# Kernel optimization log

Measured on AMD Instinct MI355X. Metric: run time of the kernel, lower is better.

## Reference

```python
import jax, jax.numpy as jnp
import numpy as np

B, C, H, W = 2, 192, 64, 64
NHEADS = 8


def setup_inputs() -> dict:
    key = jax.random.key(0)
    ks = jax.random.split(key, 6)
    L = H * W
    return {
        "x": jax.random.normal(ks[0], (B, C, H, W), dtype=jnp.float32),
        "mask": jax.random.normal(ks[1], (B, L, L), dtype=jnp.float32),
        "w_qkv": jax.random.normal(ks[2], (3 * C, C), dtype=jnp.float32) * (1.0 / np.sqrt(C)),
        "b_qkv": jax.random.normal(ks[3], (3 * C,), dtype=jnp.float32) * 0.02,
        "w_proj": jax.random.normal(ks[4], (C, C), dtype=jnp.float32) * (1.0 / np.sqrt(C)),
        "b_proj": jax.random.normal(ks[5], (C,), dtype=jnp.float32) * 0.02,
        "num_heads": NHEADS,
    }


def reference(x, mask, w_qkv, b_qkv, w_proj, b_proj, num_heads):
    b, c, h, w = x.shape
    L = h * w
    hd = c // num_heads  # head dim
    # 1x1 conv == per-pixel linear over channels
    qkv = jnp.einsum('bchw,oc->bohw', x, w_qkv) + b_qkv[None, :, None, None]
    q, k, v = jnp.split(qkv, 3, axis=1)  # each [b, c, h, w]

    def to_heads(t):
        # b (head hd) h w -> b head (h w) hd
        return t.reshape(b, num_heads, hd, L).transpose(0, 1, 3, 2)

    q, k, v = to_heads(q), to_heads(k), to_heads(v)
    scale = num_heads ** (-0.5)  # NOTE: original scales by num_heads, not head_dim
    attn = jnp.einsum('bnld,bnmd->bnlm', q, k) * scale + mask[:, None, :, :]
    attn = jax.nn.softmax(attn, axis=-1)
    out = jnp.einsum('bnlm,bnmd->bnld', attn, v)  # [b, head, L, hd]
    # b head L hd -> b (head hd) h w
    out = out.transpose(0, 1, 3, 2).reshape(b, c, h, w)
    out = jnp.einsum('bchw,oc->bohw', out, w_proj) + b_proj[None, :, None, None]
    return out
```

## Files before the change

### kernel.cpp

```cpp
#include <hip/hip_runtime.h>

#define B_  2
#define C_  192
#define L_  4096
#define NH_ 8
#define HD_ 24
#define C3_ 576
#define KV_ 64
#define NSPL_ 4
#define LSPL_ (L_ / NSPL_)
#define NTS_ (LSPL_ / KV_)
#define HG_ 4
#define KSTR_ 20

typedef _Float16 f16;
typedef __attribute__((ext_vector_type(8))) f16 f16x8;
typedef __attribute__((ext_vector_type(16))) float f32x16;

#define L2E_ 1.4426950408889634f

__device__ __forceinline__ int pk2(float a, float b) {
    union { __fp16 h __attribute__((ext_vector_type(2))); int i; } u;
    u.h = __builtin_amdgcn_cvt_pkrtz(a, b);
    return u.i;
}
__device__ __forceinline__ int pk2_rte(float a, float b) {
    union { f16 h[2]; int i; } u;
    u.h[0] = (f16)a; u.h[1] = (f16)b;
    return u.i;
}
__device__ __forceinline__ float ex2(float x) {
    float r;
    asm("v_exp_f32 %0, %1" : "=v"(r) : "v"(x));
    return r;
}
__device__ __forceinline__ float lg2(float x) {
    float r;
    asm("v_log_f32 %0, %1" : "=v"(r) : "v"(x));
    return r;
}

union Frag { f16x8 v; int i[4]; };

#define MFMA32(A, Bx, Cc) __builtin_amdgcn_mfma_f32_32x32x16_f16((A), (Bx), (Cc), 0, 0, 0)

__global__ __launch_bounds__(256) void lin_qkv(const float* __restrict__ a,
                                               const float* __restrict__ w,
                                               const float* __restrict__ bias,
                                               unsigned int* __restrict__ q2,
                                               unsigned int* __restrict__ k2t,
                                               unsigned short* __restrict__ v16) {
    __shared__ float wl[8][C_];
    const int og  = blockIdx.x;
    const int b   = blockIdx.y >> 4;
    const int lt  = blockIdx.y & 15;
    const int tid = threadIdx.x;

    for (int e = tid; e < 8 * C_; e += 256) wl[e / C_][e % C_] = w[og * 8 * C_ + e];
    __syncthreads();

    const int l = lt * 256 + tid;
    float acc[8];
#pragma unroll
    for (int j = 0; j < 8; ++j) acc[j] = bias[og * 8 + j];

    const float* ap = a + (size_t)b * C_ * L_ + l;
#pragma unroll 2
    for (int c = 0; c < C_; ++c) {
        const float xv = ap[(size_t)c * L_];
#pragma unroll
        for (int j = 0; j < 8; ++j) acc[j] = fmaf(wl[j][c], xv, acc[j]);
    }

    const float qscale = 0.35355339059327373f * L2E_;
    if (og < 24) {
        const int h = og / 3, j0 = (og % 3) * 4;
        unsigned int* p = q2 + ((size_t)(b * NH_ + h) * 12 + j0) * L_ + l;
#pragma unroll
        for (int j = 0; j < 4; ++j)
            p[(size_t)j * L_] = pk2_rte(acc[2 * j] * qscale, acc[2 * j + 1] * qscale);
    } else if (og < 48) {
        const int og_ = og - 24;
        const int h = og_ / 3, j0 = (og_ % 3) * 4;
        unsigned int* p = k2t + ((size_t)(b * NH_ + h) * L_ + l) * KSTR_ + j0;
        int4 v;
        v.x = pk2_rte(acc[0], acc[1]); v.y = pk2_rte(acc[2], acc[3]);
        v.z = pk2_rte(acc[4], acc[5]); v.w = pk2_rte(acc[6], acc[7]);
        *(int4*)p = v;
        if (j0 == 8) {
            int4 z; z.x = z.y = z.z = z.w = 0;
            *(int4*)(p + 4) = z;
            *(int4*)(p + 8) = z;
        }
    } else {
        const int og_ = og - 48;
        const int h = og_ / 3, d0 = (og_ % 3) * 8;
        unsigned short* p = v16 + ((size_t)(b * NH_ + h) * 32 + d0) * L_ + l;
#pragma unroll
        for (int j = 0; j < 8; ++j) {
            union { f16 hf; unsigned short us; } cv;
            cv.hf = (f16)acc[j];
            p[(size_t)j * L_] = cv.us;
        }
    }
}

__global__ __launch_bounds__(256) void lin_kernel(const float* __restrict__ a,
                                                  const float* __restrict__ w,
                                                  const float* __restrict__ bias,
                                                  float* __restrict__ out, int OC) {
    __shared__ float wl[8][C_];
    const int og  = blockIdx.x;
    const int b   = blockIdx.y >> 4;
    const int lt  = blockIdx.y & 15;
    const int tid = threadIdx.x;

    for (int e = tid; e < 8 * C_; e += 256) wl[e / C_][e % C_] = w[og * 8 * C_ + e];
    __syncthreads();

    const int l = lt * 256 + tid;
    float acc[8];
#pragma unroll
    for (int j = 0; j < 8; ++j) acc[j] = bias[og * 8 + j];

    const float* ap = a + (size_t)b * C_ * L_ + l;
#pragma unroll 2
    for (int c = 0; c < C_; ++c) {
        const float xv = ap[(size_t)c * L_];
#pragma unroll
        for (int j = 0; j < 8; ++j) acc[j] = fmaf(wl[j][c], xv, acc[j]);
    }

    float* op = out + ((size_t)b * OC + og * 8) * L_ + l;
#pragma unroll
    for (int j = 0; j < 8; ++j) op[(size_t)j * L_] = acc[j];
}

__global__ __launch_bounds__(256) void attn_mfma(const unsigned int* __restrict__ q2,
                                                 const unsigned int* __restrict__ k2t,
                                                 const unsigned short* __restrict__ v16,
                                                 const float* __restrict__ mask,
                                                 unsigned short* __restrict__ po,
                                                 float* __restrict__ pms) {
    const int tid  = threadIdx.x;
    const int lane = tid & 63;
    const int wid  = tid >> 6;
    const int hi   = lane >> 5;
    const int lq   = lane & 31;
    const int bid  = blockIdx.x;
    const int qt   = bid & 31;
    const int r    = bid >> 5;
    const int b    = r & 1;
    const int hg   = (r >> 1) & 1;
    const int sp   = r >> 2;
    const int qrow = qt * 128 + wid * 32 + lq;
    const int kv0  = sp * LSPL_;
    const int hbase = hg * HG_;

    const unsigned int*   qb  = q2  + (size_t)(b * NH_ + hbase) * 12 * L_;
    const int*            kb0 = (const int*)k2t + (size_t)(b * NH_ + hbase) * L_ * KSTR_;
    const unsigned short* vb0 = v16 + (size_t)(b * NH_ + hbase) * 32 * L_;
    const float* mrow = mask + ((size_t)b * L_ + qrow) * L_;

    int bq[HG_][8];
#pragma unroll
    for (int H = 0; H < HG_; ++H)
#pragma unroll
        for (int s = 0; s < 2; ++s)
#pragma unroll
            for (int t = 0; t < 4; ++t) {
                const int dpq = 8 * s + 4 * hi + t;
                bq[H][s * 4 + t] = (dpq < 12) ? qb[(size_t)(H * 12 + dpq) * L_ + qrow] : 0;
            }

#define MLOADX(MD, KK) do {                                                   \
    const float4* mb_ = (const float4*)(mrow + (KK));                         \
    _Pragma("unroll")                                                         \
    for (int q_ = 0; q_ < 4; ++q_) {                                          \
        MD[q_]     = mb_[2 * q_ + hi];                                        \
        MD[4 + q_] = mb_[8 + 2 * q_ + hi];                                    \
    } } while (0)

#define QKH(H, KK, C0, C1) do {                                               \
    Frag qf0, qf1, ka;                                                        \
    _Pragma("unroll")                                                         \
    for (int t_ = 0; t_ < 4; ++t_) { qf0.i[t_] = bq[H][t_]; qf1.i[t_] = bq[H][4 + t_]; } \
    const int* kb_ = kb0 + (size_t)(H) * L_ * KSTR_;                          \
    ka.v = *(const f16x8*)(kb_ + (size_t)((KK) + lq) * KSTR_ + 4 * hi);       \
    C0 = MFMA32(ka.v, qf0.v, mr0);                                            \
    ka.v = *(const f16x8*)(kb_ + (size_t)((KK) + lq) * KSTR_ + 8 + 4 * hi);   \
    C0 = MFMA32(ka.v, qf1.v, C0);                                             \
    ka.v = *(const f16x8*)(kb_ + (size_t)((KK) + 32 + lq) * KSTR_ + 4 * hi);  \
    C1 = MFMA32(ka.v, qf0.v, mr1);                                            \
    ka.v = *(const f16x8*)(kb_ + (size_t)((KK) + 32 + lq) * KSTR_ + 8 + 4 * hi); \
    C1 = MFMA32(ka.v, qf1.v, C1);                                             \
    } while (0)

#define SMH(H, C0, C1) do {                                                   \
    float m8[8], m4[4], m2[2];                                                \
    _Pragma("unroll")                                                         \
    for (int i_ = 0; i_ < 8; ++i_)                                            \
        m8[i_] = fmaxf(fmaxf(C0[i_], C0[i_ + 8]), fmaxf(C1[i_], C1[i_ + 8])); \
    _Pragma("unroll")                                                         \
    for (int i_ = 0; i_ < 4; ++i_) m4[i_] = fmaxf(m8[i_], m8[i_ + 4]);        \
    m2[0] = fmaxf(m4[0], m4[2]); m2[1] = fmaxf(m4[1], m4[3]);                 \
    float pmax = fmaxf(m2[0], m2[1]);                                         \
    pmax = fmaxf(pmax, __shfl_xor(pmax, 32));                                 \
    const float newm_ = fmaxf(mrun[H], pmax);                                 \
    const float r_ = ex2(mrun[H] - newm_);                                    \
    mrun[H] = newm_;                                                          \
    srun[H] *= r_;                                                            \
    _Pragma("unroll")                                                         \
    for (int i_ = 0; i_ < 16; ++i_) o[H][i_] *= r_;                           \
    _Pragma("unroll")                                                         \
    for (int i_ = 0; i_ < 16; ++i_) C0[i_] = ex2(C0[i_] - newm_);             \
    _Pragma("unroll")                                                         \
    for (int i_ = 0; i_ < 16; ++i_) C1[i_] = ex2(C1[i_] - newm_);             \
    float s8[8], s4[4];                                                       \
    _Pragma("unroll")                                                         \
    for (int i_ = 0; i_ < 8; ++i_)                                            \
        s8[i_] = (C0[i_] + C0[i_ + 8]) + (C1[i_] + C1[i_ + 8]);               \
    _Pragma("unroll")                                                         \
    for (int i_ = 0; i_ < 4; ++i_) s4[i_] = s8[i_] + s8[i_ + 4];              \
    float ls = (s4[0] + s4[2]) + (s4[1] + s4[3]);                             \
    ls += __shfl_xor(ls, 32);                                                 \
    srun[H] += ls;                                                            \
    } while (0)

#define PVH(H, KK, C0, C1) do {                                               \
    int wa1[4], wa2[4], sa1[4], sa2[4];                                       \
    int wb1[4], wb2[4], sb1[4], sb2[4];                                       \
    _Pragma("unroll")                                                         \
    for (int q_ = 0; q_ < 4; ++q_) {                                          \
        wa1[q_] = pk2(C0[4 * q_], C0[4 * q_ + 1]);                            \
        wa2[q_] = pk2(C0[4 * q_ + 2], C0[4 * q_ + 3]);                        \
        wb1[q_] = pk2(C1[4 * q_], C1[4 * q_ + 1]);                            \
        wb2[q_] = pk2(C1[4 * q_ + 2], C1[4 * q_ + 3]);                        \
    }                                                                         \
    _Pragma("unroll")                                                         \
    for (int q_ = 0; q_ < 4; ++q_) {                                          \
        sa1[q_] = __shfl_xor(wa1[q_], 32); sa2[q_] = __shfl_xor(wa2[q_], 32); \
        sb1[q_] = __shfl_xor(wb1[q_], 32); sb2[q_] = __shfl_xor(wb2[q_], 32); \
    }                                                                         \
    const unsigned short* vb_ = vb0 + (size_t)(H) * 32 * L_ + (size_t)lq * L_ + (KK) + 8 * hi; \
    _Pragma("unroll")                                                         \
    for (int s_ = 0; s_ < 2; ++s_) {                                          \
        const int qq_ = 2 * s_ + hi;                                          \
        Frag pb, va;                                                          \
        pb.i[0] = hi ? sa1[qq_] : wa1[qq_];                                   \
        pb.i[1] = hi ? sa2[qq_] : wa2[qq_];                                   \
        pb.i[2] = hi ? wa1[qq_] : sa1[qq_];                                   \
        pb.i[3] = hi ? wa2[qq_] : sa2[qq_];                                   \
        va.v = *(const f16x8*)(vb_ + 16 * s_);                                \
        o[H] = MFMA32(va.v, pb.v, o[H]);                                      \
        pb.i[0] = hi ? sb1[qq_] : wb1[qq_];                                   \
        pb.i[1] = hi ? sb2[qq_] : wb2[qq_];                                   \
        pb.i[2] = hi ? wb1[qq_] : sb1[qq_];                                   \
        pb.i[3] = hi ? wb2[qq_] : sb2[qq_];                                   \
        va.v = *(const f16x8*)(vb_ + 32 + 16 * s_);                           \
        o[H] = MFMA32(va.v, pb.v, o[H]);                                      \
    } } while (0)

#define COMPUTE(KK, MC) do {                                                  \
    f32x16 mr0, mr1;                                                          \
    _Pragma("unroll")                                                         \
    for (int q_ = 0; q_ < 4; ++q_) {                                          \
        mr0[4 * q_ + 0] = MC[q_].x * L2E_; mr0[4 * q_ + 1] = MC[q_].y * L2E_; \
        mr0[4 * q_ + 2] = MC[q_].z * L2E_; mr0[4 * q_ + 3] = MC[q_].w * L2E_; \
        mr1[4 * q_ + 0] = MC[4 + q_].x * L2E_; mr1[4 * q_ + 1] = MC[4 + q_].y * L2E_; \
        mr1[4 * q_ + 2] = MC[4 + q_].z * L2E_; mr1[4 * q_ + 3] = MC[4 + q_].w * L2E_; \
    }                                                                         \
    f32x16 cA0, cA1, cB0, cB1;                                                \
    QKH(0, KK, cA0, cA1);                                                     \
    QKH(1, KK, cB0, cB1);                                                     \
    SMH(0, cA0, cA1);                                                         \
    SMH(1, cB0, cB1);                                                         \
    PVH(0, KK, cA0, cA1);                                                     \
    PVH(1, KK, cB0, cB1);                                                     \
    QKH(2, KK, cA0, cA1);                                                     \
    QKH(3, KK, cB0, cB1);                                                     \
    SMH(2, cA0, cA1);                                                         \
    SMH(3, cB0, cB1);                                                         \
    PVH(2, KK, cA0, cA1);                                                     \
    PVH(3, KK, cB0, cB1);                                                     \
    } while (0)

    f32x16 o[HG_];
    float mrun[HG_], srun[HG_];
#pragma unroll
    for (int H = 0; H < HG_; ++H) {
#pragma unroll
        for (int i = 0; i < 16; ++i) o[H][i] = 0.f;
        mrun[H] = -1e30f;
        srun[H] = 0.f;
    }
    float4 mc[8], mn[8];

    MLOADX(mc, kv0);

#pragma clang loop unroll(disable)
    for (int t = 0; t < NTS_; t += 2) {
        const int kk = kv0 + t * KV_;
        MLOADX(mn, kk + KV_);
        COMPUTE(kk, mc);
        if (t + 2 < NTS_) MLOADX(mc, kk + 2 * KV_);
        COMPUTE(kk + KV_, mn);
    }

#pragma unroll
    for (int H = 0; H < HG_; ++H) {
        const float inv = 1.f / srun[H];
        const float lse = mrun[H] + lg2(srun[H]);
        unsigned short* pob = po + ((size_t)((sp * B_ + b) * NH_ + hbase + H) * HD_) * L_ + qrow;
#pragma unroll
        for (int i = 0; i < 16; ++i) {
            const int d = (i & 3) + 8 * (i >> 2) + 4 * hi;
            if (d < HD_) {
                union { __fp16 hf; unsigned short us; } cv;
                cv.hf = (__fp16)(o[H][i] * inv);
                pob[(size_t)d * L_] = cv.us;
            }
        }
        if (hi == 0)
            pms[((size_t)(sp * B_ + b) * NH_ + hbase + H) * L_ + qrow] = lse;
    }
#undef MLOADX
#undef QKH
#undef SMH
#undef PVH
#undef COMPUTE
}

__global__ __launch_bounds__(256) void combine_kernel(const unsigned short* __restrict__ po,
                                                      const float* __restrict__ pms,
                                                      float* __restrict__ att) {
    const int qrow = blockIdx.x * 256 + threadIdx.x;
    const int h    = blockIdx.y;
    const int b    = blockIdx.z;

    float l[NSPL_];
#pragma unroll
    for (int s = 0; s < NSPL_; ++s)
        l[s] = pms[((size_t)(s * B_ + b) * NH_ + h) * L_ + qrow];
    float lm = l[0];
#pragma unroll
    for (int s = 1; s < NSPL_; ++s) lm = fmaxf(lm, l[s]);
    float wv[NSPL_], wsum = 0.f;
#pragma unroll
    for (int s = 0; s < NSPL_; ++s) { wv[s] = ex2(l[s] - lm); wsum += wv[s]; }
    const float inv = 1.f / wsum;

    float* op = att + ((size_t)b * C_ + h * HD_) * L_ + qrow;
#pragma unroll
    for (int d = 0; d < HD_; ++d) {
        float acc = 0.f;
#pragma unroll
        for (int s = 0; s < NSPL_; ++s) {
            union { unsigned short us; __fp16 hf; } cv;
            cv.us = po[(((size_t)(s * B_ + b) * NH_ + h) * HD_ + d) * L_ + qrow];
            acc += (float)cv.hf * wv[s];
        }
        op[(size_t)d * L_] = acc * inv;
    }
}

extern "C" void kernel_launch(void* const* d_in, const int* in_sizes, int n_in,
                              void* d_out, int out_size, void* d_ws, size_t ws_size,
                              hipStream_t stream) {
    const float* x      = (const float*)d_in[0];
    const float* mask   = (const float*)d_in[1];
    const float* w_qkv  = (const float*)d_in[2];
    const float* b_qkv  = (const float*)d_in[3];
    const float* w_proj = (const float*)d_in[4];
    const float* b_proj = (const float*)d_in[5];
    float* out = (float*)d_out;

    unsigned int*   q2  = (unsigned int*)d_ws;
    unsigned int*   k2t = q2 + (size_t)B_ * NH_ * 12 * L_;
    unsigned short* v16 = (unsigned short*)(k2t + (size_t)B_ * NH_ * L_ * KSTR_);
    unsigned short* po  = v16 + (size_t)B_ * NH_ * 32 * L_;
    float* pms    = (float*)(po + (size_t)NSPL_ * B_ * NH_ * HD_ * L_);
    float* ws_att = pms + (size_t)NSPL_ * B_ * NH_ * L_;

    lin_qkv<<<dim3(72, 32), 256, 0, stream>>>(x, w_qkv, b_qkv, q2, k2t, v16);
    attn_mfma<<<dim3(512), 256, 0, stream>>>(q2, k2t, v16, mask, po, pms);
    combine_kernel<<<dim3(16, NH_, B_), 256, 0, stream>>>(po, pms, ws_att);
    lin_kernel<<<dim3(24, 32), 256, 0, stream>>>(ws_att, w_proj, b_proj, out, C_);
}
```

Baseline: 366.7 us.

## Stage mask tiles into LDS with async global_load_lds and double buffering

Mask tiles are now loaded cooperatively with coalesced 16-byte global_load_lds transfers into a double-buffered, XOR-swizzled LDS buffer. Previously each lane read its own mask row directly into registers. The aim is better coalescing of the dominant mask stream and fewer registers than the two register prefetch buffers. In exchange it adds 64KB of LDS per block, which may limit occupancy, and a __syncthreads every KV tile.

```diff
diff --git a/kernel.cpp b/kernel.cpp
--- a/kernel.cpp
+++ b/kernel.cpp
@@ -43,6 +43,14 @@
 union Frag { f16x8 v; int i[4]; };
 
 #define MFMA32(A, Bx, Cc) __builtin_amdgcn_mfma_f32_32x32x16_f16((A), (Bx), (Cc), 0, 0, 0)
+
+__device__ __forceinline__ void gload16(const void* g, void* lds) {
+    typedef const unsigned int __attribute__((address_space(1))) as1u;
+    typedef unsigned int __attribute__((address_space(3))) as3u;
+    __builtin_amdgcn_global_load_lds((as1u*)g,
+                                     (as3u*)(unsigned int)(unsigned long long)lds,
+                                     16, 0, 0);
+}
 
 __global__ __launch_bounds__(256) void lin_qkv(const float* __restrict__ a,
                                                const float* __restrict__ w,
@@ -157,10 +165,15 @@
     const int kv0  = sp * LSPL_;
     const int hbase = hg * HG_;
 
+    __shared__ __attribute__((aligned(16))) int mask_lds[2][128 * 64];
+
     const unsigned int*   qb  = q2  + (size_t)(b * NH_ + hbase) * 12 * L_;
     const int*            kb0 = (const int*)k2t + (size_t)(b * NH_ + hbase) * L_ * KSTR_;
     const unsigned short* vb0 = v16 + (size_t)(b * NH_ + hbase) * 32 * L_;
-    const float* mrow = mask + ((size_t)b * L_ + qrow) * L_;
+
+    const int mr_lo  = wid * 4 + (lane >> 4);
+    const int mchunk = (lane & 15) ^ (mr_lo & 7);
+    const float* mg = mask + ((size_t)(b * L_ + qt * 128 + mr_lo)) * L_ + mchunk * 4;
 
     int bq[HG_][8];
 #pragma unroll
@@ -173,13 +186,12 @@
                 bq[H][s * 4 + t] = (dpq < 12) ? qb[(size_t)(H * 12 + dpq) * L_ + qrow] : 0;
             }
 
-#define MLOADX(MD, KK) do {                                                   \
-    const float4* mb_ = (const float4*)(mrow + (KK));                         \
-    _Pragma("unroll")                                                         \
-    for (int q_ = 0; q_ < 4; ++q_) {                                          \
-        MD[q_]     = mb_[2 * q_ + hi];                                        \
-        MD[4 + q_] = mb_[8 + 2 * q_ + hi];                                    \
-    } } while (0)
+#define STAGEM(BF, KK) do {                                                   \
+    _Pragma("unroll")                                                         \
+    for (int j_ = 0; j_ < 8; ++j_)                                            \
+        gload16(mg + (size_t)j_ * 16 * L_ + (KK),                             \
+                (char*)&mask_lds[BF][0] + j_ * 4096 + wid * 1024);            \
+    } while (0)
 
 #define QKH(H, KK, C0, C1) do {                                               \
     Frag qf0, qf1, ka;                                                        \
@@ -261,14 +273,18 @@
         o[H] = MFMA32(va.v, pb.v, o[H]);                                      \
     } } while (0)
 
-#define COMPUTE(KK, MC) do {                                                  \
+#define COMPUTE(BF, KK) do {                                                  \
     f32x16 mr0, mr1;                                                          \
+    const int mrb_ = (wid * 32 + lq) * 64;                                    \
+    const int sw_  = (lq & 7) << 2;                                           \
     _Pragma("unroll")                                                         \
     for (int q_ = 0; q_ < 4; ++q_) {                                          \
-        mr0[4 * q_ + 0] = MC[q_].x * L2E_; mr0[4 * q_ + 1] = MC[q_].y * L2E_; \
-        mr0[4 * q_ + 2] = MC[q_].z * L2E_; mr0[4 * q_ + 3] = MC[q_].w * L2E_; \
-        mr1[4 * q_ + 0] = MC[4 + q_].x * L2E_; mr1[4 * q_ + 1] = MC[4 + q_].y * L2E_; \
-        mr1[4 * q_ + 2] = MC[4 + q_].z * L2E_; mr1[4 * q_ + 3] = MC[4 + q_].w * L2E_; \
+        const float4 a_ = *(const float4*)&mask_lds[BF][mrb_ + (((2 * q_ + hi) << 2) ^ sw_)]; \
+        mr0[4 * q_ + 0] = a_.x * L2E_; mr0[4 * q_ + 1] = a_.y * L2E_;         \
+        mr0[4 * q_ + 2] = a_.z * L2E_; mr0[4 * q_ + 3] = a_.w * L2E_;         \
+        const float4 b_ = *(const float4*)&mask_lds[BF][mrb_ + (((8 + 2 * q_ + hi) << 2) ^ sw_)]; \
+        mr1[4 * q_ + 0] = b_.x * L2E_; mr1[4 * q_ + 1] = b_.y * L2E_;         \
+        mr1[4 * q_ + 2] = b_.z * L2E_; mr1[4 * q_ + 3] = b_.w * L2E_;         \
     }                                                                         \
     f32x16 cA0, cA1, cB0, cB1;                                                \
     QKH(0, KK, cA0, cA1);                                                     \
@@ -294,17 +310,16 @@
         mrun[H] = -1e30f;
         srun[H] = 0.f;
     }
-    float4 mc[8], mn[8];
-
-    MLOADX(mc, kv0);
+
+    STAGEM(0, kv0);
+    __syncthreads();
 
 #pragma clang loop unroll(disable)
-    for (int t = 0; t < NTS_; t += 2) {
+    for (int t = 0; t < NTS_; ++t) {
         const int kk = kv0 + t * KV_;
-        MLOADX(mn, kk + KV_);
-        COMPUTE(kk, mc);
-        if (t + 2 < NTS_) MLOADX(mc, kk + 2 * KV_);
-        COMPUTE(kk + KV_, mn);
+        if (t + 1 < NTS_) STAGEM((t + 1) & 1, kk + KV_);
+        COMPUTE(t & 1, kk);
+        __syncthreads();
     }
 
 #pragma unroll
@@ -324,7 +339,7 @@
         if (hi == 0)
             pms[((size_t)(sp * B_ + b) * NH_ + hbase + H) * L_ + qrow] = lse;
     }
-#undef MLOADX
+#undef STAGEM
 #undef QKH
 #undef SMH
 #undef PVH
```

New measurement: 393.7 us. 1.07x slower.
